# Kernel tuning notes

Measured on AMD Instinct MI355X. Metric: run time of the kernel, lower is better.

## Reference

```python
import jax, jax.numpy as jnp
import numpy as np

EMBED_DIM = 1024
NUM_HEADS = 16
HEAD_DIM = EMBED_DIM // NUM_HEADS


def setup_inputs() -> dict:
    key = jax.random.key(0)
    k1, k2, k3, k4, k5 = jax.random.split(key, 5)
    B, N, C = 4, 2048, EMBED_DIM
    s = 1.0 / np.sqrt(C)
    return {
        "x": jax.random.normal(k1, (B, N, C), dtype=jnp.float32),
        "w_qkv": jax.random.uniform(k2, (C, 3 * C), dtype=jnp.float32, minval=-s, maxval=s),
        "b_qkv": jax.random.uniform(k3, (3 * C,), dtype=jnp.float32, minval=-s, maxval=s),
        "w_out": jax.random.uniform(k4, (C, C), dtype=jnp.float32, minval=-s, maxval=s),
        "b_out": jax.random.uniform(k5, (C,), dtype=jnp.float32, minval=-s, maxval=s),
    }


def reference(x, w_qkv, b_qkv, w_out, b_out):
    B, N, C = x.shape
    H, D = NUM_HEADS, HEAD_DIM
    qkv = x @ w_qkv + b_qkv                       # [B, N, 3C]
    qkv = qkv.reshape(B, N, 3, H, D)
    q = qkv[:, :, 0].transpose(0, 2, 1, 3)        # [B, H, N, D]
    k = qkv[:, :, 1].transpose(0, 2, 1, 3)
    v = qkv[:, :, 2].transpose(0, 2, 1, 3)
    scale = 1.0 / np.sqrt(D).astype(np.float32)
    attn = jnp.einsum('bhnd,bhmd->bhnm', q, k) * scale  # [B, H, N, N]
    attn = jax.nn.softmax(attn, axis=-1)
    out = jnp.einsum('bhnm,bhmd->bhnd', attn, v)  # [B, H, N, D]
    out = out.transpose(0, 2, 1, 3).reshape(B, N, C)
    return out @ w_out + b_out
```

## Files before the change

kernel.cpp:

```cpp
#include <hip/hip_runtime.h>


typedef unsigned short u16;
typedef unsigned long long u64;
typedef __bf16 bf16x8 __attribute__((ext_vector_type(8)));
typedef float f32x4 __attribute__((ext_vector_type(4)));

#define MFMA(a, b, c) __builtin_amdgcn_mfma_f32_16x16x32_bf16(a, b, c, 0, 0, 0)

__device__ __forceinline__ u16 f2bf(float f) {
    __bf16 h = (__bf16)f;
    return *(u16*)&h;
}

__device__ __forceinline__ void gld16(const void* g, void* l) {
    __builtin_amdgcn_global_load_lds(
        (const __attribute__((address_space(1))) void*)g,
        (__attribute__((address_space(3))) void*)l, 16, 0, 0);
}

__device__ __forceinline__ void lds_fence_wave() {
    __asm__ volatile("s_waitcnt lgkmcnt(0)" ::: "memory");
}

__global__ __launch_bounds__(256) void cvt_f32_bf16(
    const float* __restrict__ src, u16* __restrict__ dst, long n)
{
    long i = ((long)blockIdx.x * 256 + threadIdx.x) * 8;
    if (i >= n) return;
    float4 a = *(const float4*)&src[i];
    float4 b = *(const float4*)&src[i + 4];
    union { u16 u[8]; uint4 v; } tmp;
    tmp.u[0] = f2bf(a.x); tmp.u[1] = f2bf(a.y);
    tmp.u[2] = f2bf(a.z); tmp.u[3] = f2bf(a.w);
    tmp.u[4] = f2bf(b.x); tmp.u[5] = f2bf(b.y);
    tmp.u[6] = f2bf(b.z); tmp.u[7] = f2bf(b.w);
    *(uint4*)&dst[i] = tmp.v;
}

__global__ __launch_bounds__(256) void transpose_f2b(
    const float* __restrict__ src, u16* __restrict__ dst, int R, int C)
{
    __shared__ alignas(16) u16 tile[64 * 80];
    const int r0 = blockIdx.y * 64, c0 = blockIdx.x * 64;
    const int t = threadIdx.x;
#pragma unroll
    for (int c = 0; c < 4; c++) {
        int idx = t + c * 256;
        int r = idx >> 4, seg = idx & 15;
        float4 f = *(const float4*)&src[(long)(r0 + r) * C + c0 + seg * 4];
        u16* p = &tile[r * 80 + seg * 4];
        p[0] = f2bf(f.x); p[1] = f2bf(f.y); p[2] = f2bf(f.z); p[3] = f2bf(f.w);
    }
    __syncthreads();
#pragma unroll
    for (int c = 0; c < 2; c++) {
        int idx = t + c * 256;
        int rr = idx >> 3, seg = idx & 7;
        union { u16 u[8]; uint4 v; } tmp;
#pragma unroll
        for (int j = 0; j < 8; j++) tmp.u[j] = tile[(seg * 8 + j) * 80 + rr];
        *(uint4*)&dst[(long)(c0 + rr) * R + r0 + seg * 8] = tmp.v;
    }
}

template <int EPI>
__global__ __launch_bounds__(256) void gemm_bf16(
    const u16* __restrict__ A, const u16* __restrict__ Bt,
    const float* __restrict__ bias,
    u16* __restrict__ out0, u16* __restrict__ out1, u16* __restrict__ out2,
    float* __restrict__ outf,
    int M, int N, int K)
{
    const int m0 = blockIdx.x * 128, n0 = blockIdx.y * 128;
    const int t = threadIdx.x;
    const int wave = t >> 6, lane = t & 63, quad = lane >> 4, l15 = lane & 15;
    const int wm = wave >> 1, wn = wave & 1;

    __shared__ alignas(16) u16 As[128 * 64];
    __shared__ alignas(16) u16 Bs[128 * 64];

    const int srow = wave * 32 + (lane >> 3);
    const int scol = (((lane & 7) ^ (lane >> 3)) & 7) * 8;

    f32x4 acc[4][4] = {};

    for (int k0 = 0; k0 < K; k0 += 64) {
        __syncthreads();
#pragma unroll
        for (int c = 0; c < 4; c++) {
            gld16(&A[(long)(m0 + srow + c * 8) * K + k0 + scol],
                  &As[(wave * 32 + c * 8) * 64]);
            gld16(&Bt[(long)(n0 + srow + c * 8) * K + k0 + scol],
                  &Bs[(wave * 32 + c * 8) * 64]);
        }
        __syncthreads();

#pragma unroll
        for (int ks = 0; ks < 2; ks++) {
            bf16x8 af[4], bf[4];
#pragma unroll
            for (int mt = 0; mt < 4; mt++) {
                int row = wm * 64 + mt * 16 + l15;
                af[mt] = *(bf16x8*)&As[row * 64 + (((ks * 4 + quad) ^ (row & 7)) * 8)];
            }
#pragma unroll
            for (int nt = 0; nt < 4; nt++) {
                int row = wn * 64 + nt * 16 + l15;
                bf[nt] = *(bf16x8*)&Bs[row * 64 + (((ks * 4 + quad) ^ (row & 7)) * 8)];
            }
#pragma unroll
            for (int mt = 0; mt < 4; mt++)
#pragma unroll
                for (int nt = 0; nt < 4; nt++)
                    acc[mt][nt] = MFMA(bf[nt], af[mt], acc[mt][nt]);
        }
    }

#pragma unroll
    for (int mt = 0; mt < 4; mt++) {
        int token = m0 + wm * 64 + mt * 16 + l15;
        int bb = token >> 11, nn = token & 2047;
#pragma unroll
        for (int nt = 0; nt < 4; nt++) {
            int cgb = n0 + wn * 64 + nt * 16 + quad * 4;
            float4 bv = *(const float4*)&bias[cgb];
            float v0 = acc[mt][nt][0] + bv.x;
            float v1 = acc[mt][nt][1] + bv.y;
            float v2 = acc[mt][nt][2] + bv.z;
            float v3 = acc[mt][nt][3] + bv.w;
            if (EPI == 0) {
                int t3 = cgb >> 10;
                int hh = (cgb >> 6) & 15, dd = cgb & 63;
                int bh = (bb << 4) + hh;
                if (t3 == 0) {
                    union { u16 u[4]; u64 v; } pk;
                    pk.u[0] = f2bf(v0 * 0.125f); pk.u[1] = f2bf(v1 * 0.125f);
                    pk.u[2] = f2bf(v2 * 0.125f); pk.u[3] = f2bf(v3 * 0.125f);
                    *(u64*)&out0[((long)bh * 2048 + nn) * 64 + dd] = pk.v;
                } else if (t3 == 1) {
                    union { u16 u[4]; u64 v; } pk;
                    pk.u[0] = f2bf(v0); pk.u[1] = f2bf(v1);
                    pk.u[2] = f2bf(v2); pk.u[3] = f2bf(v3);
                    *(u64*)&out1[((long)bh * 2048 + nn) * 64 + dd] = pk.v;
                } else {
                    long vbo = ((long)bh * 64 + dd) * 2048 + nn;
                    out2[vbo]            = f2bf(v0);
                    out2[vbo + 2048]     = f2bf(v1);
                    out2[vbo + 2 * 2048] = f2bf(v2);
                    out2[vbo + 3 * 2048] = f2bf(v3);
                }
            } else {
                float4 o4 = { v0, v1, v2, v3 };
                *(float4*)&outf[(long)token * N + cgb] = o4;
            }
        }
    }
}

__global__ __launch_bounds__(256, 3) void flash_attn(
    const u16* __restrict__ q, const u16* __restrict__ k,
    const u16* __restrict__ vt, u16* __restrict__ attn)
{
    const int bh = blockIdx.y;
    const int b = bh >> 4, h = bh & 15;
    const int q0 = blockIdx.x * 128;
    const int t = threadIdx.x;
    const int wave = t >> 6, lane = t & 63, quad = lane >> 4, l15 = lane & 15;

    __shared__ alignas(16) u16 Ks[2][4096];
    __shared__ alignas(16) u16 Vs[2][4096];
    __shared__ alignas(16) __bf16 Ps[128 * 72];

    const u16* kb = k + (long)bh * 2048 * 64;
    const u16* vb = vt + (long)bh * 64 * 2048;

    bf16x8 qf[2][2];
#pragma unroll
    for (int mt = 0; mt < 2; mt++) {
        long row = (long)bh * 2048 + q0 + wave * 32 + mt * 16 + l15;
        qf[mt][0] = *(const bf16x8*)&q[row * 64 + quad * 8];
        qf[mt][1] = *(const bf16x8*)&q[row * 64 + 32 + quad * 8];
    }

    bf16x8 ones;
#pragma unroll
    for (int j = 0; j < 8; j++) ones[j] = (__bf16)1.0f;

    const int ri = lane >> 3;
    const int ci = (lane & 7) ^ ri;
    const int s0 = wave * 2;

    const int sw0 = ((quad ^ (l15 & 7)) * 8);
    const int prow = (wave * 32 + l15) * 72;

    f32x4 o[2][4] = {};
    f32x4 ls[2] = {};

#pragma unroll
    for (int c = 0; c < 2; c++) {
        int s = s0 + c;
        gld16(&kb[(long)(s * 8 + ri) * 64 + ci * 8], &Ks[0][s * 512]);
        gld16(&vb[(long)(s * 8 + ri) * 2048 + ci * 8], &Vs[0][s * 512]);
    }

    for (int kt = 0; kt < 32; kt++) {
        const int cur = kt & 1;
        __syncthreads();

        if (kt < 31) {
#pragma unroll
            for (int c = 0; c < 2; c++) {
                int s = s0 + c;
                gld16(&kb[(long)((kt + 1) * 64 + s * 8 + ri) * 64 + ci * 8],
                      &Ks[cur ^ 1][s * 512]);
                gld16(&vb[(long)(s * 8 + ri) * 2048 + (kt + 1) * 64 + ci * 8],
                      &Vs[cur ^ 1][s * 512]);
            }
        }

        f32x4 st[2][4];
#pragma unroll
        for (int ct = 0; ct < 4; ct++) {
            const u16* kr = &Ks[cur][(ct * 16 + l15) * 64];
            bf16x8 kf0 = *(const bf16x8*)&kr[sw0];
            bf16x8 kf1 = *(const bf16x8*)&kr[sw0 ^ 32];
#pragma unroll
            for (int mt = 0; mt < 2; mt++) {
                f32x4 z = {};
                z = MFMA(kf0, qf[mt][0], z);
                st[mt][ct] = MFMA(kf1, qf[mt][1], z);
            }
        }

#pragma unroll
        for (int mt = 0; mt < 2; mt++)
#pragma unroll
            for (int ct = 0; ct < 4; ct++) {
                union { u16 u[4]; u64 v; } pk;
#pragma unroll
                for (int r = 0; r < 4; r++)
                    pk.u[r] = f2bf(__expf(st[mt][ct][r]));
                *(u64*)&Ps[prow + mt * 16 * 72 + ct * 16 + quad * 4] = pk.v;
            }
        lds_fence_wave();

        bf16x8 pb[2][2];
#pragma unroll
        for (int mt = 0; mt < 2; mt++) {
            pb[mt][0] = *(bf16x8*)&Ps[prow + mt * 16 * 72 + quad * 8];
            pb[mt][1] = *(bf16x8*)&Ps[prow + mt * 16 * 72 + 32 + quad * 8];
            ls[mt] = MFMA(ones, pb[mt][0], ls[mt]);
            ls[mt] = MFMA(ones, pb[mt][1], ls[mt]);
        }
#pragma unroll
        for (int dt = 0; dt < 4; dt++) {
            const u16* vr = &Vs[cur][(dt * 16 + l15) * 64];
            bf16x8 va0 = *(const bf16x8*)&vr[sw0];
            bf16x8 va1 = *(const bf16x8*)&vr[sw0 ^ 32];
#pragma unroll
            for (int mt = 0; mt < 2; mt++) {
                o[mt][dt] = MFMA(va0, pb[mt][0], o[mt][dt]);
                o[mt][dt] = MFMA(va1, pb[mt][1], o[mt][dt]);
            }
        }
    }

#pragma unroll
    for (int mt = 0; mt < 2; mt++) {
        float inv = 1.f / ls[mt][0];
        int n = q0 + wave * 32 + mt * 16 + l15;
#pragma unroll
        for (int dt = 0; dt < 4; dt++) {
            union { u16 u[4]; u64 v; } pk;
#pragma unroll
            for (int r = 0; r < 4; r++) pk.u[r] = f2bf(o[mt][dt][r] * inv);
            *(u64*)&attn[((long)b * 2048 + n) * 1024 + h * 64 + dt * 16 + quad * 4] =
                pk.v;
        }
    }
}

extern "C" void kernel_launch(void* const* d_in, const int* in_sizes, int n_in,
                              void* d_out, int out_size, void* d_ws, size_t ws_size,
                              hipStream_t stream) {
    const float* x     = (const float*)d_in[0];
    const float* w_qkv = (const float*)d_in[1];
    const float* b_qkv = (const float*)d_in[2];
    const float* w_out = (const float*)d_in[3];
    const float* b_out = (const float*)d_in[4];
    float* out = (float*)d_out;

    u16* ws    = (u16*)d_ws;
    u16* q     = ws;
    u16* kk    = q + 8388608;
    u16* vt    = kk + 8388608;
    u16* attn  = vt + 8388608;
    u16* x_bf  = attn + 8388608;
    u16* wqkvT = x_bf + 8388608;
    u16* woutT = wqkvT + 3145728;

    cvt_f32_bf16<<<4096, 256, 0, stream>>>(x, x_bf, 8388608L);
    transpose_f2b<<<dim3(48, 16), 256, 0, stream>>>(w_qkv, wqkvT, 1024, 3072);
    transpose_f2b<<<dim3(16, 16), 256, 0, stream>>>(w_out, woutT, 1024, 1024);
    gemm_bf16<0><<<dim3(64, 24), 256, 0, stream>>>(x_bf, wqkvT, b_qkv, q, kk, vt,
                                                   nullptr, 8192, 3072, 1024);
    flash_attn<<<dim3(16, 64), 256, 0, stream>>>(q, kk, vt, attn);
    gemm_bf16<1><<<dim3(64, 8), 256, 0, stream>>>(attn, woutT, b_out, nullptr,
                                                  nullptr, nullptr, out,
                                                  8192, 1024, 1024);
}
```

Measured before the change: 277.9 us.

## Replace LDS round-trip for P with permlane32 swaps and permuted K rows

The attention kernel no longer writes exponentiated scores to a shared-memory P buffer and reads them back as MFMA operands. It permutes which K rows each lane loads, so the score accumulator layout lines up with the B-operand layout, and uses permlane32_swap to exchange halves across lanes in registers. Dropping the P buffer cuts LDS use and LDS traffic, and the launch bound is raised from 3 to 4 blocks per SIMD to use the freed space. The risk is extra register pressure under the tighter bound, and correctness depends on the lane permutation matching exactly.

Result: faster. 271.6 us (-2.2%).

```diff
diff --git a/kernel.cpp b/kernel.cpp
--- a/kernel.cpp
+++ b/kernel.cpp
@@ -5,6 +5,7 @@
 typedef unsigned long long u64;
 typedef __bf16 bf16x8 __attribute__((ext_vector_type(8)));
 typedef float f32x4 __attribute__((ext_vector_type(4)));
+typedef unsigned int u32x2 __attribute__((ext_vector_type(2)));
 
 #define MFMA(a, b, c) __builtin_amdgcn_mfma_f32_16x16x32_bf16(a, b, c, 0, 0, 0)
 
@@ -17,10 +18,6 @@
     __builtin_amdgcn_global_load_lds(
         (const __attribute__((address_space(1))) void*)g,
         (__attribute__((address_space(3))) void*)l, 16, 0, 0);
-}
-
-__device__ __forceinline__ void lds_fence_wave() {
-    __asm__ volatile("s_waitcnt lgkmcnt(0)" ::: "memory");
 }
 
 __global__ __launch_bounds__(256) void cvt_f32_bf16(
@@ -158,7 +155,7 @@
     }
 }
 
-__global__ __launch_bounds__(256, 3) void flash_attn(
+__global__ __launch_bounds__(256, 4) void flash_attn(
     const u16* __restrict__ q, const u16* __restrict__ k,
     const u16* __restrict__ vt, u16* __restrict__ attn)
 {
@@ -170,7 +167,6 @@
 
     __shared__ alignas(16) u16 Ks[2][4096];
     __shared__ alignas(16) u16 Vs[2][4096];
-    __shared__ alignas(16) __bf16 Ps[128 * 72];
 
     const u16* kb = k + (long)bh * 2048 * 64;
     const u16* vb = vt + (long)bh * 64 * 2048;
@@ -189,17 +185,18 @@
 
     const int ri = lane >> 3;
     const int ci = (lane & 7) ^ ri;
-    const int s0 = wave * 2;
-
-    const int sw0 = ((quad ^ (l15 & 7)) * 8);
-    const int prow = (wave * 32 + l15) * 72;
+    const int sg = wave * 2;
+
+    const int lperm = (l15 & 3) | ((l15 & 4) << 1) | ((l15 & 8) >> 1);
+    const int swk = (quad ^ (lperm & 7)) * 8;
+    const int swv = (quad ^ (l15 & 7)) * 8;
 
     f32x4 o[2][4] = {};
     f32x4 ls[2] = {};
 
 #pragma unroll
     for (int c = 0; c < 2; c++) {
-        int s = s0 + c;
+        int s = sg + c;
         gld16(&kb[(long)(s * 8 + ri) * 64 + ci * 8], &Ks[0][s * 512]);
         gld16(&vb[(long)(s * 8 + ri) * 2048 + ci * 8], &Vs[0][s * 512]);
     }
@@ -211,7 +208,7 @@
         if (kt < 31) {
 #pragma unroll
             for (int c = 0; c < 2; c++) {
-                int s = s0 + c;
+                int s = sg + c;
                 gld16(&kb[(long)((kt + 1) * 64 + s * 8 + ri) * 64 + ci * 8],
                       &Ks[cur ^ 1][s * 512]);
                 gld16(&vb[(long)(s * 8 + ri) * 2048 + (kt + 1) * 64 + ci * 8],
@@ -222,9 +219,9 @@
         f32x4 st[2][4];
 #pragma unroll
         for (int ct = 0; ct < 4; ct++) {
-            const u16* kr = &Ks[cur][(ct * 16 + l15) * 64];
-            bf16x8 kf0 = *(const bf16x8*)&kr[sw0];
-            bf16x8 kf1 = *(const bf16x8*)&kr[sw0 ^ 32];
+            const u16* kr = &Ks[cur][(ct * 16 + lperm) * 64];
+            bf16x8 kf0 = *(const bf16x8*)&kr[swk];
+            bf16x8 kf1 = *(const bf16x8*)&kr[swk ^ 32];
 #pragma unroll
             for (int mt = 0; mt < 2; mt++) {
                 f32x4 z = {};
@@ -233,31 +230,44 @@
             }
         }
 
-#pragma unroll
-        for (int mt = 0; mt < 2; mt++)
-#pragma unroll
-            for (int ct = 0; ct < 4; ct++) {
-                union { u16 u[4]; u64 v; } pk;
-#pragma unroll
-                for (int r = 0; r < 4; r++)
-                    pk.u[r] = f2bf(__expf(st[mt][ct][r]));
-                *(u64*)&Ps[prow + mt * 16 * 72 + ct * 16 + quad * 4] = pk.v;
-            }
-        lds_fence_wave();
-
         bf16x8 pb[2][2];
 #pragma unroll
         for (int mt = 0; mt < 2; mt++) {
-            pb[mt][0] = *(bf16x8*)&Ps[prow + mt * 16 * 72 + quad * 8];
-            pb[mt][1] = *(bf16x8*)&Ps[prow + mt * 16 * 72 + 32 + quad * 8];
+            unsigned w[4][2];
+#pragma unroll
+            for (int ct = 0; ct < 4; ct++)
+#pragma unroll
+                for (int p = 0; p < 2; p++) {
+                    u16 lo = f2bf(__expf(st[mt][ct][2 * p]));
+                    u16 hi = f2bf(__expf(st[mt][ct][2 * p + 1]));
+                    w[ct][p] = (unsigned)lo | ((unsigned)hi << 16);
+                }
+#pragma unroll
+            for (int hh = 0; hh < 2; hh++) {
+                u32x2 pa0 = __builtin_amdgcn_permlane32_swap(
+                    w[2 * hh][0], w[2 * hh + 1][0], false, false);
+                u32x2 pa1 = __builtin_amdgcn_permlane32_swap(
+                    w[2 * hh][1], w[2 * hh + 1][1], false, false);
+                union { unsigned d[4]; bf16x8 v; } uu;
+                uu.d[0] = pa0[0];
+                uu.d[1] = pa1[0];
+                uu.d[2] = pa0[1];
+                uu.d[3] = pa1[1];
+                pb[mt][hh] = uu.v;
+            }
+        }
+
+#pragma unroll
+        for (int mt = 0; mt < 2; mt++) {
             ls[mt] = MFMA(ones, pb[mt][0], ls[mt]);
             ls[mt] = MFMA(ones, pb[mt][1], ls[mt]);
         }
+
 #pragma unroll
         for (int dt = 0; dt < 4; dt++) {
             const u16* vr = &Vs[cur][(dt * 16 + l15) * 64];
-            bf16x8 va0 = *(const bf16x8*)&vr[sw0];
-            bf16x8 va1 = *(const bf16x8*)&vr[sw0 ^ 32];
+            bf16x8 va0 = *(const bf16x8*)&vr[swv];
+            bf16x8 va1 = *(const bf16x8*)&vr[swv ^ 32];
 #pragma unroll
             for (int mt = 0; mt < 2; mt++) {
                 o[mt][dt] = MFMA(va0, pb[mt][0], o[mt][dt]);
```
